# Kernel tuning notes

Measured on AMD Instinct MI355X. Metric: run time of the kernel, lower is better.

## Reference

```python
import jax, jax.numpy as jnp
import numpy as np

B, N, C, H = 2, 2048, 1024, 16
HD = C // H  # head dim 64
SCALE = HD ** -0.5


def setup_inputs() -> dict:
    key = jax.random.key(0)
    ks = jax.random.split(key, 5)
    x = jax.random.normal(ks[0], (B, N, C), dtype=jnp.float32)
    padding_mask = jax.random.randint(ks[1], (B, N), 0, 2).astype(jnp.bool_)
    alibi_bias = jax.random.normal(ks[2], (B, H, N, N), dtype=jnp.float32)
    qkv_w = jax.random.normal(ks[3], (3 * C, C), dtype=jnp.float32) * (C ** -0.5)
    proj_w = jax.random.normal(ks[4], (C, C), dtype=jnp.float32) * (C ** -0.5)
    proj_b = jnp.zeros((C,), dtype=jnp.float32)
    return {"x": x, "padding_mask": padding_mask, "alibi_bias": alibi_bias,
            "qkv_w": qkv_w, "proj_w": proj_w, "proj_b": proj_b}


def reference(x, padding_mask, alibi_bias, qkv_w, proj_w, proj_b):
    b, n, c = x.shape
    # qkv projection (torch Linear: x @ W^T), split into q,k,v heads
    qkv = (x @ qkv_w.T).reshape(b, n, 3, H, HD)
    qkv = jnp.transpose(qkv, (2, 0, 3, 1, 4))  # [3, B, H, N, HD]
    q, k, v = qkv[0], qkv[1], qkv[2]
    # scaled QK^T + alibi bias
    attn = jnp.einsum("bhqd,bhkd->bhqk", q * SCALE, k) + alibi_bias
    # padding mask over keys -> -inf
    attn = jnp.where(padding_mask[:, None, None, :], -jnp.inf, attn)
    # softmax in fp32, cast back
    attn = jax.nn.softmax(attn.astype(jnp.float32), axis=-1).astype(x.dtype)
    # AV, merge heads, output projection
    out = jnp.einsum("bhqk,bhkd->bqhd", attn, v).reshape(b, n, c)
    return out @ proj_w.T + proj_b
```

## Files before the change

kernel.cpp:

```cpp
#include <hip/hip_runtime.h>
#include <hip/hip_bf16.h>


typedef short bf16x8 __attribute__((ext_vector_type(8)));
typedef float f32x4 __attribute__((ext_vector_type(4)));

#define NB 2
#define NSEQ 2048
#define NC 1024
#define NH 16
#define NHD 64

__device__ __forceinline__ unsigned short f2bf(float f) {
    unsigned int u = __float_as_uint(f);
    u += 0x7fffu + ((u >> 16) & 1u);
    return (unsigned short)(u >> 16);
}
__device__ __forceinline__ float bf2f(unsigned short h) {
    return __uint_as_float(((unsigned int)h) << 16);
}

__device__ __forceinline__ void cvt_store(const float4 v, unsigned short* dh, unsigned short* dl) {
    unsigned short h0 = f2bf(v.x), h1 = f2bf(v.y), h2 = f2bf(v.z), h3 = f2bf(v.w);
    unsigned short l0 = f2bf(v.x - bf2f(h0)), l1 = f2bf(v.y - bf2f(h1));
    unsigned short l2 = f2bf(v.z - bf2f(h2)), l3 = f2bf(v.w - bf2f(h3));
    uint2 hp, lp;
    hp.x = (unsigned)h0 | ((unsigned)h1 << 16); hp.y = (unsigned)h2 | ((unsigned)h3 << 16);
    lp.x = (unsigned)l0 | ((unsigned)l1 << 16); lp.y = (unsigned)l2 | ((unsigned)l3 << 16);
    *(uint2*)dh = hp;
    *(uint2*)dl = lp;
}

template <int EPI>
__global__ __launch_bounds__(256) void gemm_split(
    const float* __restrict__ A, const float* __restrict__ Bm,
    unsigned short* __restrict__ qws, unsigned short* __restrict__ kws,
    unsigned short* __restrict__ vws,
    float* __restrict__ outp, const float* __restrict__ bias)
{
    __shared__ unsigned short Ah[64][40], Al[64][40], Bh[64][40], Bl[64][40];
    const int t = threadIdx.x;
    const int wave = t >> 6, lane = t & 63;
    const int lrow = lane & 15, quad = lane >> 4;
    const int rowBase = blockIdx.y * 64;
    const int colBase = blockIdx.x * 64;

    f32x4 acc[4];
    #pragma unroll
    for (int i = 0; i < 4; i++) acc[i] = (f32x4){0.f, 0.f, 0.f, 0.f};

    for (int kt = 0; kt < 1024; kt += 32) {
        __syncthreads();
        #pragma unroll
        for (int i = 0; i < 2; i++) {
            int idx = t + i * 256;
            int row = idx >> 3;
            int col4 = (idx & 7) * 4;
            float4 av = *(const float4*)&A[(size_t)(rowBase + row) * 1024 + kt + col4];
            float4 bv = *(const float4*)&Bm[(size_t)(colBase + row) * 1024 + kt + col4];
            cvt_store(av, &Ah[row][col4], &Al[row][col4]);
            cvt_store(bv, &Bh[row][col4], &Bl[row][col4]);
        }
        __syncthreads();

        bf16x8 ah = *(const bf16x8*)&Ah[wave * 16 + lrow][quad * 8];
        bf16x8 al = *(const bf16x8*)&Al[wave * 16 + lrow][quad * 8];
        #pragma unroll
        for (int nt = 0; nt < 4; nt++) {
            bf16x8 bh = *(const bf16x8*)&Bh[nt * 16 + lrow][quad * 8];
            bf16x8 bl = *(const bf16x8*)&Bl[nt * 16 + lrow][quad * 8];
            acc[nt] = __builtin_amdgcn_mfma_f32_16x16x32_bf16(ah, bh, acc[nt], 0, 0, 0);
            acc[nt] = __builtin_amdgcn_mfma_f32_16x16x32_bf16(al, bh, acc[nt], 0, 0, 0);
            acc[nt] = __builtin_amdgcn_mfma_f32_16x16x32_bf16(ah, bl, acc[nt], 0, 0, 0);
        }
    }

    const int m0 = rowBase + wave * 16 + quad * 4;
    if (EPI == 0) {
        #pragma unroll
        for (int nt = 0; nt < 4; nt++) {
            int ncol = colBase + nt * 16 + lrow;
            int three = ncol >> 10;
            int hh = (ncol >> 6) & 15;
            int d = ncol & 63;
            unsigned short* dst = (three == 0) ? qws : ((three == 1) ? kws : vws);
            float sc = (three == 0) ? 0.125f : 1.0f;
            #pragma unroll
            for (int r = 0; r < 4; r++) {
                int m = m0 + r;
                int bb = m >> 11, nn = m & 2047;
                dst[(((size_t)(bb * NH + hh)) * NSEQ + nn) * NHD + d] = f2bf(acc[nt][r] * sc);
            }
        }
    } else {
        #pragma unroll
        for (int nt = 0; nt < 4; nt++) {
            int ncol = colBase + nt * 16 + lrow;
            float bv = bias[ncol];
            #pragma unroll
            for (int r = 0; r < 4; r++) {
                outp[(size_t)(m0 + r) * 1024 + ncol] = acc[nt][r] + bv;
            }
        }
    }
}

__global__ __launch_bounds__(256) void attn_fused(
    const unsigned short* __restrict__ qws, const unsigned short* __restrict__ kws,
    const unsigned short* __restrict__ vws,
    const float* __restrict__ alibi, const int* __restrict__ mask,
    float* __restrict__ attn_out)
{
    __shared__ unsigned short Klds[32][72];
    __shared__ unsigned short Vt[64][40];
    __shared__ unsigned short Plds[4][16][40];

    const int t = threadIdx.x;
    const int wave = t >> 6, lane = t & 63;
    const int lrow = lane & 15, quad = lane >> 4;
    const int bh = blockIdx.y;
    const int b = bh >> 4;
    const int q0 = blockIdx.x * 64;

    const size_t qkvbase = (size_t)bh * NSEQ * NHD;

    const int qrow = q0 + wave * 16 + lrow;
    bf16x8 qf0 = *(const bf16x8*)&qws[qkvbase + (size_t)qrow * NHD + quad * 8];
    bf16x8 qf1 = *(const bf16x8*)&qws[qkvbase + (size_t)qrow * NHD + 32 + quad * 8];

    float mrow[4], lsum[4];
    f32x4 acc[4];
    #pragma unroll
    for (int r = 0; r < 4; r++) { mrow[r] = -1e30f; lsum[r] = 0.f; }
    #pragma unroll
    for (int i = 0; i < 4; i++) acc[i] = (f32x4){0.f, 0.f, 0.f, 0.f};

    const float* alibi_b = alibi + ((size_t)bh * NSEQ + q0 + wave * 16) * NSEQ;
    const int* mask_b = mask + b * NSEQ;

    for (int kk0 = 0; kk0 < NSEQ; kk0 += 32) {
        {
            int key = t >> 3;
            int dcol = (t & 7) * 8;
            *(uint4*)&Klds[key][dcol] =
                *(const uint4*)&kws[qkvbase + (size_t)(kk0 + key) * NHD + dcol];
            unsigned short vv[8];
            *(uint4*)vv = *(const uint4*)&vws[qkvbase + (size_t)(kk0 + key) * NHD + dcol];
            #pragma unroll
            for (int i = 0; i < 8; i++) Vt[dcol + i][key] = vv[i];
        }
        __syncthreads();

        f32x4 s0 = (f32x4){0.f, 0.f, 0.f, 0.f};
        f32x4 s1 = (f32x4){0.f, 0.f, 0.f, 0.f};
        {
            bf16x8 k0a = *(const bf16x8*)&Klds[lrow][quad * 8];
            bf16x8 k0b = *(const bf16x8*)&Klds[lrow][32 + quad * 8];
            s0 = __builtin_amdgcn_mfma_f32_16x16x32_bf16(qf0, k0a, s0, 0, 0, 0);
            s0 = __builtin_amdgcn_mfma_f32_16x16x32_bf16(qf1, k0b, s0, 0, 0, 0);
            bf16x8 k1a = *(const bf16x8*)&Klds[16 + lrow][quad * 8];
            bf16x8 k1b = *(const bf16x8*)&Klds[16 + lrow][32 + quad * 8];
            s1 = __builtin_amdgcn_mfma_f32_16x16x32_bf16(qf0, k1a, s1, 0, 0, 0);
            s1 = __builtin_amdgcn_mfma_f32_16x16x32_bf16(qf1, k1b, s1, 0, 0, 0);
        }

        const int key0 = kk0 + lrow, key1 = kk0 + 16 + lrow;
        const int msk0 = mask_b[key0], msk1 = mask_b[key1];
        #pragma unroll
        for (int r = 0; r < 4; r++) {
            size_t aoff = (size_t)(quad * 4 + r) * NSEQ;
            float v0 = msk0 ? -1e30f : (s0[r] + alibi_b[aoff + key0]);
            float v1 = msk1 ? -1e30f : (s1[r] + alibi_b[aoff + key1]);
            float mx = fmaxf(v0, v1);
            mx = fmaxf(mx, __shfl_xor(mx, 1, 64));
            mx = fmaxf(mx, __shfl_xor(mx, 2, 64));
            mx = fmaxf(mx, __shfl_xor(mx, 4, 64));
            mx = fmaxf(mx, __shfl_xor(mx, 8, 64));
            float mn = fmaxf(mrow[r], mx);
            float alpha = __expf(mrow[r] - mn);
            mrow[r] = mn;
            float p0 = __expf(v0 - mn);
            float p1 = __expf(v1 - mn);
            float ps = p0 + p1;
            ps += __shfl_xor(ps, 1, 64);
            ps += __shfl_xor(ps, 2, 64);
            ps += __shfl_xor(ps, 4, 64);
            ps += __shfl_xor(ps, 8, 64);
            lsum[r] = lsum[r] * alpha + ps;
            #pragma unroll
            for (int nt = 0; nt < 4; nt++) acc[nt][r] *= alpha;
            Plds[wave][quad * 4 + r][lrow] = f2bf(p0);
            Plds[wave][quad * 4 + r][16 + lrow] = f2bf(p1);
        }

        {
            bf16x8 pf = *(const bf16x8*)&Plds[wave][lrow][quad * 8];
            #pragma unroll
            for (int nt = 0; nt < 4; nt++) {
                bf16x8 vf = *(const bf16x8*)&Vt[nt * 16 + lrow][quad * 8];
                acc[nt] = __builtin_amdgcn_mfma_f32_16x16x32_bf16(pf, vf, acc[nt], 0, 0, 0);
            }
        }
        __syncthreads();
    }

    const int h = bh & 15;
    #pragma unroll
    for (int nt = 0; nt < 4; nt++) {
        #pragma unroll
        for (int r = 0; r < 4; r++) {
            float inv = 1.f / lsum[r];
            attn_out[(size_t)(b * NSEQ + q0 + wave * 16 + quad * 4 + r) * NC
                     + h * 64 + nt * 16 + lrow] = acc[nt][r] * inv;
        }
    }
}

extern "C" void kernel_launch(void* const* d_in, const int* in_sizes, int n_in,
                              void* d_out, int out_size, void* d_ws, size_t ws_size,
                              hipStream_t stream) {
    const float* x      = (const float*)d_in[0];
    const int*   mask   = (const int*)d_in[1];
    const float* alibi  = (const float*)d_in[2];
    const float* qkv_w  = (const float*)d_in[3];
    const float* proj_w = (const float*)d_in[4];
    const float* proj_b = (const float*)d_in[5];
    float* out = (float*)d_out;

    char* w = (char*)d_ws;
    unsigned short* qws = (unsigned short*)(w);
    unsigned short* kws = (unsigned short*)(w + 8388608);
    unsigned short* vws = (unsigned short*)(w + 16777216);
    float* attn_out     = (float*)(w + 25165824);

    gemm_split<0><<<dim3(48, 64), 256, 0, stream>>>(x, qkv_w, qws, kws, vws, nullptr, nullptr);
    attn_fused<<<dim3(32, 32), 256, 0, stream>>>(qws, kws, vws, alibi, mask, attn_out);
    gemm_split<1><<<dim3(16, 64), 256, 0, stream>>>(attn_out, proj_w, nullptr, nullptr, nullptr, out, proj_b);
}
```

Before: 1.147 ms.

## Pre-convert operands to interleaved bf16 pairs, enlarge GEMM tiles, double-buffer attention loads

Adds conversion kernels that turn x and both weight matrices into interleaved hi/lo bf16 pairs, so the GEMMs stream pre-converted data with global_load_lds over a K of 2048. The weights use a duplicated-high layout, which drops their low-part term. The GEMMs move to 128-row tiles with 4x(BN/32) MFMA blocking. The attention kernel stores V transposed, double-buffers 64-key K/V tiles through global_load_lds, prefetches alibi and mask a step ahead, and writes bf16 hi/lo output for the projection GEMM. This cuts the per-tile conversion work and load latency, at the cost of extra conversion launches and workspace traffic.

```diff
diff --git a/kernel.cpp b/kernel.cpp
--- a/kernel.cpp
+++ b/kernel.cpp
@@ -5,11 +5,8 @@
 typedef short bf16x8 __attribute__((ext_vector_type(8)));
 typedef float f32x4 __attribute__((ext_vector_type(4)));
 
-#define NB 2
 #define NSEQ 2048
-#define NC 1024
 #define NH 16
-#define NHD 64
 
 __device__ __forceinline__ unsigned short f2bf(float f) {
     unsigned int u = __float_as_uint(f);
@@ -20,86 +17,120 @@
     return __uint_as_float(((unsigned int)h) << 16);
 }
 
-__device__ __forceinline__ void cvt_store(const float4 v, unsigned short* dh, unsigned short* dl) {
-    unsigned short h0 = f2bf(v.x), h1 = f2bf(v.y), h2 = f2bf(v.z), h3 = f2bf(v.w);
-    unsigned short l0 = f2bf(v.x - bf2f(h0)), l1 = f2bf(v.y - bf2f(h1));
-    unsigned short l2 = f2bf(v.z - bf2f(h2)), l3 = f2bf(v.w - bf2f(h3));
-    uint2 hp, lp;
-    hp.x = (unsigned)h0 | ((unsigned)h1 << 16); hp.y = (unsigned)h2 | ((unsigned)h3 << 16);
-    lp.x = (unsigned)l0 | ((unsigned)l1 << 16); lp.y = (unsigned)l2 | ((unsigned)l3 << 16);
-    *(uint2*)dh = hp;
-    *(uint2*)dl = lp;
-}
-
-template <int EPI>
-__global__ __launch_bounds__(256) void gemm_split(
-    const float* __restrict__ A, const float* __restrict__ Bm,
-    unsigned short* __restrict__ qws, unsigned short* __restrict__ kws,
-    unsigned short* __restrict__ vws,
-    float* __restrict__ outp, const float* __restrict__ bias)
+__device__ __forceinline__ void gll16(const void* g, void* l) {
+    __builtin_amdgcn_global_load_lds(
+        (const __attribute__((address_space(1))) unsigned int*)g,
+        (__attribute__((address_space(3))) unsigned int*)l, 16, 0, 0);
+}
+
+__global__ __launch_bounds__(256) void conv2(const float* __restrict__ in,
+                                             unsigned short* __restrict__ outp,
+                                             int n4, int dup) {
+    int i = blockIdx.x * 256 + threadIdx.x;
+    if (i >= n4) return;
+    float4 v = ((const float4*)in)[i];
+    float vs[4] = {v.x, v.y, v.z, v.w};
+    unsigned r[4];
+    #pragma unroll
+    for (int j = 0; j < 4; ++j) {
+        unsigned short hh = f2bf(vs[j]);
+        unsigned short ll = dup ? hh : f2bf(vs[j] - bf2f(hh));
+        r[j] = (unsigned)hh | ((unsigned)ll << 16);
+    }
+    uint4 pk; pk.x = r[0]; pk.y = r[1]; pk.z = r[2]; pk.w = r[3];
+    *(uint4*)&outp[(size_t)i * 8] = pk;
+}
+
+template <int EPI, int BN>
+__global__ __launch_bounds__(256) void gemm2k(
+    const unsigned short* __restrict__ A2, const unsigned short* __restrict__ B2,
+    unsigned short* __restrict__ qo, unsigned short* __restrict__ ko,
+    unsigned short* __restrict__ vto, float* __restrict__ outp,
+    const float* __restrict__ bias)
 {
-    __shared__ unsigned short Ah[64][40], Al[64][40], Bh[64][40], Bl[64][40];
+    constexpr int K2 = 2048;
+    constexpr int NT = BN / 32;
+    __shared__ __align__(16) unsigned short Ash[128 * 64];
+    __shared__ __align__(16) unsigned short Bsh[BN * 64];
     const int t = threadIdx.x;
     const int wave = t >> 6, lane = t & 63;
     const int lrow = lane & 15, quad = lane >> 4;
-    const int rowBase = blockIdx.y * 64;
-    const int colBase = blockIdx.x * 64;
-
-    f32x4 acc[4];
-    #pragma unroll
-    for (int i = 0; i < 4; i++) acc[i] = (f32x4){0.f, 0.f, 0.f, 0.f};
-
-    for (int kt = 0; kt < 1024; kt += 32) {
+    const int wr = wave & 1, wc = wave >> 1;
+    const int rowBase = blockIdx.y * 128;
+    const int colBase = blockIdx.x * BN;
+
+    f32x4 acc[4][NT];
+    #pragma unroll
+    for (int mt = 0; mt < 4; ++mt)
+        #pragma unroll
+        for (int nt = 0; nt < NT; ++nt)
+            acc[mt][nt] = (f32x4){0.f, 0.f, 0.f, 0.f};
+
+    const int srow = lane >> 3;
+    const int scol = (lane & 7) * 16;
+    const char* Ag = (const char*)A2 + ((size_t)(rowBase + wave * 32 + srow) * K2) * 2 + scol;
+    char* Als = (char*)Ash + (wave * 32 + srow) * 128 + scol;
+    const char* Bg = (const char*)B2 + ((size_t)(colBase + wave * (BN / 4) + srow) * K2) * 2 + scol;
+    char* Bls = (char*)Bsh + (wave * (BN / 4) + srow) * 128 + scol;
+
+    for (int kt = 0; kt < K2; kt += 64) {
         __syncthreads();
         #pragma unroll
-        for (int i = 0; i < 2; i++) {
-            int idx = t + i * 256;
-            int row = idx >> 3;
-            int col4 = (idx & 7) * 4;
-            float4 av = *(const float4*)&A[(size_t)(rowBase + row) * 1024 + kt + col4];
-            float4 bv = *(const float4*)&Bm[(size_t)(colBase + row) * 1024 + kt + col4];
-            cvt_store(av, &Ah[row][col4], &Al[row][col4]);
-            cvt_store(bv, &Bh[row][col4], &Bl[row][col4]);
-        }
+        for (int j = 0; j < 4; ++j)
+            gll16(Ag + ((size_t)j * 8 * K2 + kt) * 2, Als + j * 8 * 128);
+        #pragma unroll
+        for (int j = 0; j < BN / 32; ++j)
+            gll16(Bg + ((size_t)j * 8 * K2 + kt) * 2, Bls + j * 8 * 128);
         __syncthreads();
-
-        bf16x8 ah = *(const bf16x8*)&Ah[wave * 16 + lrow][quad * 8];
-        bf16x8 al = *(const bf16x8*)&Al[wave * 16 + lrow][quad * 8];
-        #pragma unroll
-        for (int nt = 0; nt < 4; nt++) {
-            bf16x8 bh = *(const bf16x8*)&Bh[nt * 16 + lrow][quad * 8];
-            bf16x8 bl = *(const bf16x8*)&Bl[nt * 16 + lrow][quad * 8];
-            acc[nt] = __builtin_amdgcn_mfma_f32_16x16x32_bf16(ah, bh, acc[nt], 0, 0, 0);
-            acc[nt] = __builtin_amdgcn_mfma_f32_16x16x32_bf16(al, bh, acc[nt], 0, 0, 0);
-            acc[nt] = __builtin_amdgcn_mfma_f32_16x16x32_bf16(ah, bl, acc[nt], 0, 0, 0);
-        }
-    }
-
-    const int m0 = rowBase + wave * 16 + quad * 4;
-    if (EPI == 0) {
-        #pragma unroll
-        for (int nt = 0; nt < 4; nt++) {
-            int ncol = colBase + nt * 16 + lrow;
-            int three = ncol >> 10;
-            int hh = (ncol >> 6) & 15;
-            int d = ncol & 63;
-            unsigned short* dst = (three == 0) ? qws : ((three == 1) ? kws : vws);
-            float sc = (three == 0) ? 0.125f : 1.0f;
-            #pragma unroll
-            for (int r = 0; r < 4; r++) {
-                int m = m0 + r;
-                int bb = m >> 11, nn = m & 2047;
-                dst[(((size_t)(bb * NH + hh)) * NSEQ + nn) * NHD + d] = f2bf(acc[nt][r] * sc);
-            }
-        }
-    } else {
-        #pragma unroll
-        for (int nt = 0; nt < 4; nt++) {
-            int ncol = colBase + nt * 16 + lrow;
-            float bv = bias[ncol];
-            #pragma unroll
-            for (int r = 0; r < 4; r++) {
-                outp[(size_t)(m0 + r) * 1024 + ncol] = acc[nt][r] + bv;
+        #pragma unroll
+        for (int ks = 0; ks < 2; ++ks) {
+            bf16x8 af[4], bfr[NT];
+            #pragma unroll
+            for (int mt = 0; mt < 4; ++mt)
+                af[mt] = *(const bf16x8*)&Ash[(wr * 64 + mt * 16 + lrow) * 64 + ks * 32 + quad * 8];
+            #pragma unroll
+            for (int nt = 0; nt < NT; ++nt)
+                bfr[nt] = *(const bf16x8*)&Bsh[(wc * (BN / 2) + nt * 16 + lrow) * 64 + ks * 32 + quad * 8];
+            #pragma unroll
+            for (int mt = 0; mt < 4; ++mt)
+                #pragma unroll
+                for (int nt = 0; nt < NT; ++nt)
+                    acc[mt][nt] = __builtin_amdgcn_mfma_f32_16x16x32_bf16(af[mt], bfr[nt], acc[mt][nt], 0, 0, 0);
+        }
+    }
+
+    #pragma unroll
+    for (int mt = 0; mt < 4; ++mt) {
+        const int m0 = rowBase + wr * 64 + mt * 16 + quad * 4;
+        const int bb = m0 >> 11, nn0 = m0 & 2047;
+        #pragma unroll
+        for (int nt = 0; nt < NT; ++nt) {
+            const int col = colBase + wc * (BN / 2) + nt * 16 + lrow;
+            if (EPI == 0) {
+                const int three = col >> 10;
+                const int hh2 = (col >> 6) & 15, dd = col & 63;
+                const size_t bhh = (size_t)bb * NH + hh2;
+                if (three == 0) {
+                    #pragma unroll
+                    for (int r = 0; r < 4; ++r)
+                        qo[(bhh * NSEQ + nn0 + r) * 64 + dd] = f2bf(acc[mt][nt][r] * 0.125f);
+                } else if (three == 1) {
+                    #pragma unroll
+                    for (int r = 0; r < 4; ++r)
+                        ko[(bhh * NSEQ + nn0 + r) * 64 + dd] = f2bf(acc[mt][nt][r]);
+                } else {
+                    unsigned short pk[4];
+                    #pragma unroll
+                    for (int r = 0; r < 4; ++r) pk[r] = f2bf(acc[mt][nt][r]);
+                    uint2 u; u.x = (unsigned)pk[0] | ((unsigned)pk[1] << 16);
+                    u.y = (unsigned)pk[2] | ((unsigned)pk[3] << 16);
+                    *(uint2*)&vto[(bhh * 64 + dd) * NSEQ + nn0] = u;
+                }
+            } else {
+                const float bv = bias[col];
+                #pragma unroll
+                for (int r = 0; r < 4; ++r)
+                    outp[(size_t)(m0 + r) * 1024 + col] = acc[mt][nt][r] + bv;
             }
         }
     }
@@ -107,111 +138,140 @@
 
 __global__ __launch_bounds__(256) void attn_fused(
     const unsigned short* __restrict__ qws, const unsigned short* __restrict__ kws,
-    const unsigned short* __restrict__ vws,
+    const unsigned short* __restrict__ vtws,
     const float* __restrict__ alibi, const int* __restrict__ mask,
-    float* __restrict__ attn_out)
+    unsigned short* __restrict__ ao2)
 {
-    __shared__ unsigned short Klds[32][72];
-    __shared__ unsigned short Vt[64][40];
-    __shared__ unsigned short Plds[4][16][40];
+    __shared__ __align__(16) unsigned short Klds[2][64][64];
+    __shared__ __align__(16) unsigned short Vt[2][64][64];
+    __shared__ __align__(16) unsigned short Plds[4][16][72];
 
     const int t = threadIdx.x;
     const int wave = t >> 6, lane = t & 63;
     const int lrow = lane & 15, quad = lane >> 4;
-    const int bh = blockIdx.y;
-    const int b = bh >> 4;
+    const int bh = blockIdx.y, b = bh >> 4, h = bh & 15;
     const int q0 = blockIdx.x * 64;
-
-    const size_t qkvbase = (size_t)bh * NSEQ * NHD;
+    const size_t kvbase = (size_t)bh * NSEQ * 64;
 
     const int qrow = q0 + wave * 16 + lrow;
-    bf16x8 qf0 = *(const bf16x8*)&qws[qkvbase + (size_t)qrow * NHD + quad * 8];
-    bf16x8 qf1 = *(const bf16x8*)&qws[qkvbase + (size_t)qrow * NHD + 32 + quad * 8];
+    bf16x8 qf0 = *(const bf16x8*)&qws[kvbase + (size_t)qrow * 64 + quad * 8];
+    bf16x8 qf1 = *(const bf16x8*)&qws[kvbase + (size_t)qrow * 64 + 32 + quad * 8];
+
+    const float* alibi_w = alibi + ((size_t)bh * NSEQ + q0 + wave * 16 + quad * 4) * NSEQ;
+    const int* mask_b = mask + b * NSEQ;
+
+    const int srow = lane >> 3;
+    const int scol = (lane & 7) * 16;
+
+    auto stage = [&](int kk0, int buf) {
+        #pragma unroll
+        for (int j = 0; j < 2; ++j) {
+            const int row = wave * 16 + j * 8 + srow;
+            gll16((const char*)kws + (kvbase + (size_t)(kk0 + row) * 64) * 2 + scol,
+                  (char*)&Klds[buf][0][0] + row * 128 + scol);
+            gll16((const char*)vtws + (((size_t)bh * 64 + row) * NSEQ + kk0) * 2 + scol,
+                  (char*)&Vt[buf][0][0] + row * 128 + scol);
+        }
+    };
+
+    float apf[4][4]; int mpf[4];
+    auto pref = [&](int kk0) {
+        #pragma unroll
+        for (int nt = 0; nt < 4; ++nt) {
+            const int key = kk0 + nt * 16 + lrow;
+            mpf[nt] = mask_b[key];
+            #pragma unroll
+            for (int r = 0; r < 4; ++r)
+                apf[nt][r] = alibi_w[(size_t)r * NSEQ + key];
+        }
+    };
 
     float mrow[4], lsum[4];
     f32x4 acc[4];
     #pragma unroll
-    for (int r = 0; r < 4; r++) { mrow[r] = -1e30f; lsum[r] = 0.f; }
-    #pragma unroll
-    for (int i = 0; i < 4; i++) acc[i] = (f32x4){0.f, 0.f, 0.f, 0.f};
-
-    const float* alibi_b = alibi + ((size_t)bh * NSEQ + q0 + wave * 16) * NSEQ;
-    const int* mask_b = mask + b * NSEQ;
-
-    for (int kk0 = 0; kk0 < NSEQ; kk0 += 32) {
-        {
-            int key = t >> 3;
-            int dcol = (t & 7) * 8;
-            *(uint4*)&Klds[key][dcol] =
-                *(const uint4*)&kws[qkvbase + (size_t)(kk0 + key) * NHD + dcol];
-            unsigned short vv[8];
-            *(uint4*)vv = *(const uint4*)&vws[qkvbase + (size_t)(kk0 + key) * NHD + dcol];
-            #pragma unroll
-            for (int i = 0; i < 8; i++) Vt[dcol + i][key] = vv[i];
-        }
+    for (int r = 0; r < 4; ++r) { mrow[r] = -1e30f; lsum[r] = 0.f; }
+    #pragma unroll
+    for (int i = 0; i < 4; ++i) acc[i] = (f32x4){0.f, 0.f, 0.f, 0.f};
+
+    stage(0, 0);
+    pref(0);
+
+    for (int it = 0; it < 32; ++it) {
+        const int cur = it & 1;
         __syncthreads();
-
-        f32x4 s0 = (f32x4){0.f, 0.f, 0.f, 0.f};
-        f32x4 s1 = (f32x4){0.f, 0.f, 0.f, 0.f};
-        {
-            bf16x8 k0a = *(const bf16x8*)&Klds[lrow][quad * 8];
-            bf16x8 k0b = *(const bf16x8*)&Klds[lrow][32 + quad * 8];
-            s0 = __builtin_amdgcn_mfma_f32_16x16x32_bf16(qf0, k0a, s0, 0, 0, 0);
-            s0 = __builtin_amdgcn_mfma_f32_16x16x32_bf16(qf1, k0b, s0, 0, 0, 0);
-            bf16x8 k1a = *(const bf16x8*)&Klds[16 + lrow][quad * 8];
-            bf16x8 k1b = *(const bf16x8*)&Klds[16 + lrow][32 + quad * 8];
-            s1 = __builtin_amdgcn_mfma_f32_16x16x32_bf16(qf0, k1a, s1, 0, 0, 0);
-            s1 = __builtin_amdgcn_mfma_f32_16x16x32_bf16(qf1, k1b, s1, 0, 0, 0);
-        }
-
-        const int key0 = kk0 + lrow, key1 = kk0 + 16 + lrow;
-        const int msk0 = mask_b[key0], msk1 = mask_b[key1];
-        #pragma unroll
-        for (int r = 0; r < 4; r++) {
-            size_t aoff = (size_t)(quad * 4 + r) * NSEQ;
-            float v0 = msk0 ? -1e30f : (s0[r] + alibi_b[aoff + key0]);
-            float v1 = msk1 ? -1e30f : (s1[r] + alibi_b[aoff + key1]);
-            float mx = fmaxf(v0, v1);
+        if (it < 31) stage((it + 1) * 64, cur ^ 1);
+
+        float acur[4][4]; int mcur[4];
+        #pragma unroll
+        for (int nt = 0; nt < 4; ++nt) {
+            mcur[nt] = mpf[nt];
+            #pragma unroll
+            for (int r = 0; r < 4; ++r) acur[nt][r] = apf[nt][r];
+        }
+        if (it < 31) pref((it + 1) * 64);
+
+        f32x4 s[4];
+        #pragma unroll
+        for (int nt = 0; nt < 4; ++nt) {
+            bf16x8 kf0 = *(const bf16x8*)&Klds[cur][nt * 16 + lrow][quad * 8];
+            bf16x8 kf1 = *(const bf16x8*)&Klds[cur][nt * 16 + lrow][32 + quad * 8];
+            s[nt] = (f32x4){0.f, 0.f, 0.f, 0.f};
+            s[nt] = __builtin_amdgcn_mfma_f32_16x16x32_bf16(qf0, kf0, s[nt], 0, 0, 0);
+            s[nt] = __builtin_amdgcn_mfma_f32_16x16x32_bf16(qf1, kf1, s[nt], 0, 0, 0);
+        }
+
+        #pragma unroll
+        for (int r = 0; r < 4; ++r) {
+            float vv[4];
+            #pragma unroll
+            for (int nt = 0; nt < 4; ++nt)
+                vv[nt] = mcur[nt] ? -1e30f : (s[nt][r] + acur[nt][r]);
+            float mx = fmaxf(fmaxf(vv[0], vv[1]), fmaxf(vv[2], vv[3]));
             mx = fmaxf(mx, __shfl_xor(mx, 1, 64));
             mx = fmaxf(mx, __shfl_xor(mx, 2, 64));
             mx = fmaxf(mx, __shfl_xor(mx, 4, 64));
             mx = fmaxf(mx, __shfl_xor(mx, 8, 64));
-            float mn = fmaxf(mrow[r], mx);
-            float alpha = __expf(mrow[r] - mn);
+            const float mn = fmaxf(mrow[r], mx);
+            const float alpha = __expf(mrow[r] - mn);
             mrow[r] = mn;
-            float p0 = __expf(v0 - mn);
-            float p1 = __expf(v1 - mn);
-            float ps = p0 + p1;
+            float p[4], ps = 0.f;
+            #pragma unroll
+            for (int nt = 0; nt < 4; ++nt) { p[nt] = __expf(vv[nt] - mn); ps += p[nt]; }
             ps += __shfl_xor(ps, 1, 64);
             ps += __shfl_xor(ps, 2, 64);
             ps += __shfl_xor(ps, 4, 64);
             ps += __shfl_xor(ps, 8, 64);
             lsum[r] = lsum[r] * alpha + ps;
             #pragma unroll
-            for (int nt = 0; nt < 4; nt++) acc[nt][r] *= alpha;
-            Plds[wave][quad * 4 + r][lrow] = f2bf(p0);
-            Plds[wave][quad * 4 + r][16 + lrow] = f2bf(p1);
-        }
-
-        {
-            bf16x8 pf = *(const bf16x8*)&Plds[wave][lrow][quad * 8];
-            #pragma unroll
-            for (int nt = 0; nt < 4; nt++) {
-                bf16x8 vf = *(const bf16x8*)&Vt[nt * 16 + lrow][quad * 8];
-                acc[nt] = __builtin_amdgcn_mfma_f32_16x16x32_bf16(pf, vf, acc[nt], 0, 0, 0);
-            }
-        }
-        __syncthreads();
-    }
-
-    const int h = bh & 15;
-    #pragma unroll
-    for (int nt = 0; nt < 4; nt++) {
-        #pragma unroll
-        for (int r = 0; r < 4; r++) {
-            float inv = 1.f / lsum[r];
-            attn_out[(size_t)(b * NSEQ + q0 + wave * 16 + quad * 4 + r) * NC
-                     + h * 64 + nt * 16 + lrow] = acc[nt][r] * inv;
+            for (int nt = 0; nt < 4; ++nt) acc[nt][r] *= alpha;
+            #pragma unroll
+            for (int nt = 0; nt < 4; ++nt)
+                Plds[wave][quad * 4 + r][nt * 16 + lrow] = f2bf(p[nt]);
+        }
+
+        bf16x8 pf0 = *(const bf16x8*)&Plds[wave][lrow][quad * 8];
+        bf16x8 pf1 = *(const bf16x8*)&Plds[wave][lrow][32 + quad * 8];
+        #pragma unroll
+        for (int nt = 0; nt < 4; ++nt) {
+            bf16x8 vf0 = *(const bf16x8*)&Vt[cur][nt * 16 + lrow][quad * 8];
+            bf16x8 vf1 = *(const bf16x8*)&Vt[cur][nt * 16 + lrow][32 + quad * 8];
+            acc[nt] = __builtin_amdgcn_mfma_f32_16x16x32_bf16(pf0, vf0, acc[nt], 0, 0, 0);
+            acc[nt] = __builtin_amdgcn_mfma_f32_16x16x32_bf16(pf1, vf1, acc[nt], 0, 0, 0);
+        }
+    }
+
+    #pragma unroll
+    for (int r = 0; r < 4; ++r) {
+        const float inv = 1.f / lsum[r];
+        const int m = b * NSEQ + q0 + wave * 16 + quad * 4 + r;
+        #pragma unroll
+        for (int nt = 0; nt < 4; ++nt) {
+            const float o = acc[nt][r] * inv;
+            const unsigned short hh_ = f2bf(o);
+            const unsigned short ll_ = f2bf(o - bf2f(hh_));
+            const int col = h * 64 + nt * 16 + lrow;
+            *(unsigned*)&ao2[(size_t)m * 2048 + col * 2] =
+                (unsigned)hh_ | ((unsigned)ll_ << 16);
         }
     }
 }
@@ -228,12 +288,18 @@
     float* out = (float*)d_out;
 
     char* w = (char*)d_ws;
-    unsigned short* qws = (unsigned short*)(w);
-    unsigned short* kws = (unsigned short*)(w + 8388608);
-    unsigned short* vws = (unsigned short*)(w + 16777216);
-    float* attn_out     = (float*)(w + 25165824);
-
-    gemm_split<0><<<dim3(48, 64), 256, 0, stream>>>(x, qkv_w, qws, kws, vws, nullptr, nullptr);
-    attn_fused<<<dim3(32, 32), 256, 0, stream>>>(qws, kws, vws, alibi, mask, attn_out);
-    gemm_split<1><<<dim3(16, 64), 256, 0, stream>>>(attn_out, proj_w, nullptr, nullptr, nullptr, out, proj_b);
-}
+    unsigned short* qws    = (unsigned short*)(w);
+    unsigned short* kws    = (unsigned short*)(w + 8388608);
+    unsigned short* vtws   = (unsigned short*)(w + 16777216);
+    unsigned short* x2     = (unsigned short*)(w + 25165824);
+    unsigned short* ao2    = x2;
+    unsigned short* qkvw2  = (unsigned short*)(w + 41943040);
+    unsigned short* projw2 = (unsigned short*)(w + 54525952);
+
+    conv2<<<4096, 256, 0, stream>>>(x, x2, 1048576, 0);
+    conv2<<<3072, 256, 0, stream>>>(qkv_w, qkvw2, 786432, 1);
+    conv2<<<1024, 256, 0, stream>>>(proj_w, projw2, 262144, 1);
+    gemm2k<0, 128><<<dim3(24, 32), 256, 0, stream>>>(x2, qkvw2, qws, kws, vtws, nullptr, nullptr);
+    attn_fused<<<dim3(32, 32), 256, 0, stream>>>(qws, kws, vtws, alibi, mask, ao2);
+    gemm2k<1, 64><<<dim3(16, 32), 256, 0, stream>>>(ao2, projw2, nullptr, nullptr, nullptr, out, proj_b);
+}
```

New measurement: 947.8 us. 1.21x faster.
